# Kernel optimization log

Measured on AMD Instinct MI355X. Metric: run time of the kernel, lower is better.

The kernel has to match this reference:

```python
import jax, jax.numpy as jnp
import numpy as np
from jax import lax

B, S, E, DF, H, L, V, T = 32, 512, 512, 2048, 8, 2, 30000, 12
START, STOP = 10, 11
NEG = -10000.0


def setup_inputs() -> dict:
    key = jax.random.key(0)
    ks = jax.random.split(key, 12)
    g = lambda i, shape, sc=0.02: jax.random.normal(ks[i], shape, jnp.float32) * sc
    trans = jax.random.normal(ks[9], (T, T), jnp.float32)
    trans = trans.at[START, :].set(NEG).at[:, STOP].set(NEG)
    return {
        "sentence": jax.random.randint(ks[0], (B, S), 0, V),
        "seq_len": jax.random.randint(ks[1], (B,), 1, S + 1),
        "tags": jax.random.randint(ks[2], (B, S), 0, 10),
        "emb": g(3, (V, E), 1.0),
        "attn_in_w": g(4, (L, 3 * E, E)), "attn_in_b": jnp.zeros((L, 3 * E)),
        "attn_out_w": g(5, (L, E, E)), "attn_out_b": jnp.zeros((L, E)),
        "ln1_g": jnp.ones((L, E)), "ln1_b": jnp.zeros((L, E)),
        "ln2_g": jnp.ones((L, E)), "ln2_b": jnp.zeros((L, E)),
        "ff1_w": g(6, (L, DF, E)), "ff1_b": jnp.zeros((L, DF)),
        "ff2_w": g(7, (L, E, DF)), "ff2_b": jnp.zeros((L, E)),
        "tag_w": g(8, (T, E)), "tag_b": jnp.zeros((T,)),
        "transitions": trans,
    }


def _ln(x, g, b):
    m = x.mean(-1, keepdims=True)
    v = ((x - m) ** 2).mean(-1, keepdims=True)
    return (x - m) / jnp.sqrt(v + 1e-5) * g + b


def _mha(x, w_in, b_in, w_out, b_out):
    b_, s_, e_ = x.shape
    d = e_ // H
    qkv = x @ w_in.T + b_in
    q, k, v = jnp.split(qkv, 3, axis=-1)
    split = lambda t: t.reshape(b_, s_, H, d).transpose(0, 2, 1, 3)
    q, k, v = split(q), split(k), split(v)
    att = jax.nn.softmax(jnp.einsum('bhqd,bhkd->bhqk', q, k) / np.sqrt(d).astype(np.float32), axis=-1)
    o = jnp.einsum('bhqk,bhkd->bhqd', att, v).transpose(0, 2, 1, 3).reshape(b_, s_, e_)
    return o @ w_out.T + b_out


def _forward_impl(sentence, seq_len, tags, emb, attn_in_w, attn_in_b, attn_out_w,
                  attn_out_b, ln1_g, ln1_b, ln2_g, ln2_b, ff1_w, ff1_b, ff2_w,
                  ff2_b, tag_w, tag_b, transitions):
    # Transformer encoder features (dropout in eval mode -> identity)
    x = emb[sentence]  # (B,S,E)
    for l in range(L):
        x = _ln(x + _mha(x, attn_in_w[l], attn_in_b[l], attn_out_w[l], attn_out_b[l]), ln1_g[l], ln1_b[l])
        h = jax.nn.relu(x @ ff1_w[l].T + ff1_b[l]) @ ff2_w[l].T + ff2_b[l]
        x = _ln(x + h, ln2_g[l], ln2_b[l])
    feats = x @ tag_w.T + tag_b  # (B,S,T)

    # CRF forward algorithm (log-semiring scan, masked by seq_len)
    alpha0 = jnp.full((B, T), NEG, feats.dtype).at[:, START].set(0.0)

    def step(alpha, xs):
        emit_t, t = xs  # emit_t: (B,T)
        new = emit_t + jax.nn.logsumexp(alpha[:, None, :] + transitions[None, :, :], axis=-1)
        return jnp.where((t < seq_len)[:, None], new, alpha), None

    alpha, _ = lax.scan(step, alpha0, (feats.transpose(1, 0, 2), jnp.arange(S)))
    fwd_score = jax.nn.logsumexp(alpha + transitions[STOP][None, :], axis=-1)  # (B,)

    # gold score (vectorized _score_sentence)
    tags_ext = jnp.concatenate([jnp.full((B, 1), START, tags.dtype), tags], axis=1)  # (B,S+1)
    mask = jnp.arange(S)[None, :] < seq_len[:, None]  # (B,S)
    trans_sc = jnp.where(mask, transitions[tags_ext[:, 1:], tags_ext[:, :-1]], 0.0).sum(-1)
    emit_sc = jnp.where(mask, jnp.take_along_axis(feats, tags[:, :, None], axis=2)[..., 0], 0.0).sum(-1)
    last_tag = jnp.take_along_axis(tags_ext, seq_len[:, None], axis=1)[:, 0]
    gold = trans_sc + emit_sc + transitions[STOP, last_tag]

    return jnp.mean(fwd_score - gold)


def reference(sentence, seq_len, tags, emb, attn_in_w, attn_in_b, attn_out_w,
              attn_out_b, ln1_g, ln1_b, ln2_g, ln2_b, ff1_w, ff1_b, ff2_w,
              ff2_b, tag_w, tag_b, transitions):
    return _forward_impl(sentence, seq_len, tags, emb, attn_in_w, attn_in_b,
                         attn_out_w, attn_out_b, ln1_g, ln1_b, ln2_g, ln2_b,
                         ff1_w, ff1_b, ff2_w, ff2_b, tag_w, tag_b, transitions)
```

## Files before the change

kernel.cpp:

```cpp
#include <hip/hip_runtime.h>
#include <hip/hip_bf16.h>

#define BB 32
#define SSZ 512
#define EE 512
#define DFF 2048
#define HH 8
#define LL 2
#define TT 12
#define START_TAG 10
#define STOP_TAG 11
#define CB 8
#define CM (CB * SSZ)
#define NCHUNK (BB / CB)
#define NBH (CB * HH)
#define NBH_ALL (BB * HH)
#define NCHK 8

typedef __hip_bfloat16 bf16;
typedef __attribute__((ext_vector_type(8))) short short8;
typedef __attribute__((ext_vector_type(4))) float f32x4;

__device__ __forceinline__ float b2f(bf16 x) { return __bfloat162float(x); }
__device__ __forceinline__ float ldw(const void* p, size_t i, bool isbf) {
  return isbf ? __bfloat162float(((const bf16*)p)[i]) : ((const float*)p)[i];
}

__device__ __forceinline__ void gl_lds16(const bf16* g, bf16* l) {
  __builtin_amdgcn_global_load_lds(
      (const __attribute__((address_space(1))) void*)g,
      (__attribute__((address_space(3))) void*)l, 16, 0, 0);
}

__device__ __forceinline__ int swz(int row, int col) {
  return row * 128 + (col ^ (((row >> 2) & 7) * 16));
}

__global__ void k_detect(const void* trans, int* dflag) {
  if (threadIdx.x == 0) {
    const unsigned short* u = (const unsigned short*)trans;
    dflag[0] = (u[START_TAG * TT] == 0xC61C && u[START_TAG * TT + 1] == 0xC61C) ? 1 : 0;
  }
}

__global__ void k_cvt(const void* src, bf16* dst, long n, const int* dflag) {
  bool isbf = dflag[0] != 0;
  for (long i = (long)blockIdx.x * 256 + threadIdx.x; i < n; i += (long)gridDim.x * 256)
    dst[i] = __float2bfloat16(ldw(src, i, isbf));
}

__global__ void k_embed(const int* sent, const void* emb, bf16* xb, const int* dflag) {
  bool isbf = dflag[0] != 0;
  int tok = blockIdx.x;
  int v = sent[tok];
  bf16* xo = xb + (size_t)tok * EE;
  for (int i = threadIdx.x; i < EE; i += 256)
    xo[i] = __float2bfloat16(ldw(emb, (size_t)v * EE + i, isbf));
}

__global__ __launch_bounds__(256) void k_mgemm(
    const bf16* __restrict__ A, const bf16* __restrict__ W,
    const void* __restrict__ bias, size_t boff, bf16* __restrict__ Cb,
    bf16* __restrict__ vtout, int M, int N, int K, int relu, const int* dflag) {
  bool isbf = dflag[0] != 0;
  __shared__ __align__(16) bf16 Sh[2 * 128 * 64];
  bf16* As = Sh;
  bf16* Bs = Sh + 128 * 64;
  const int tid = threadIdx.x;
  const int lane = tid & 63;
  const int wave = tid >> 6;
  const int wm = wave >> 1, wn = wave & 1;
  const int m0 = blockIdx.x * 128, n0 = blockIdx.y * 128;
  const int lrow = lane & 15, lk = lane >> 4;
  const int rl = lane >> 3, sl = lane & 7;

  f32x4 acc[4][4];
#pragma unroll
  for (int i = 0; i < 4; ++i)
#pragma unroll
    for (int j = 0; j < 4; ++j) acc[i][j] = (f32x4){0.f, 0.f, 0.f, 0.f};

  for (int kt = 0; kt < K; kt += 64) {
#pragma unroll
    for (int i = 0; i < 4; ++i) {
      int r = wave * 32 + i * 8 + rl;
      int gs = sl ^ (r & 7);
      gl_lds16(A + (size_t)(m0 + r) * K + kt + gs * 8, As + wave * 2048 + i * 512);
      gl_lds16(W + (size_t)(n0 + r) * K + kt + gs * 8, Bs + wave * 2048 + i * 512);
    }
    __syncthreads();
#pragma unroll
    for (int kb = 0; kb < 64; kb += 32) {
      short8 af[4], bfr[4];
#pragma unroll
      for (int mf = 0; mf < 4; ++mf) {
        int r = wm * 64 + mf * 16 + lrow;
        int ps = ((kb >> 3) + lk) ^ (r & 7);
        af[mf] = *(const short8*)&As[r * 64 + ps * 8];
      }
#pragma unroll
      for (int nf = 0; nf < 4; ++nf) {
        int r = wn * 64 + nf * 16 + lrow;
        int ps = ((kb >> 3) + lk) ^ (r & 7);
        bfr[nf] = *(const short8*)&Bs[r * 64 + ps * 8];
      }
#pragma unroll
      for (int mf = 0; mf < 4; ++mf)
#pragma unroll
        for (int nf = 0; nf < 4; ++nf)
          acc[mf][nf] = __builtin_amdgcn_mfma_f32_16x16x32_bf16(
              af[mf], bfr[nf], acc[mf][nf], 0, 0, 0);
    }
    __syncthreads();
  }

  const bool vpath = (vtout != nullptr) && (n0 >= 1024);
  if (!vpath) {
#pragma unroll
    for (int nf = 0; nf < 4; ++nf) {
      int nl = wn * 64 + nf * 16 + lrow;
      float bia = ldw(bias, boff + n0 + nl, isbf);
#pragma unroll
      for (int mf = 0; mf < 4; ++mf) {
#pragma unroll
        for (int r = 0; r < 4; ++r) {
          int ml = wm * 64 + mf * 16 + lk * 4 + r;
          float v = acc[mf][nf][r] + bia;
          if (relu) v = fmaxf(v, 0.f);
          Sh[swz(ml, nl)] = __float2bfloat16(v);
        }
      }
    }
    __syncthreads();
#pragma unroll
    for (int p = 0; p < 8; ++p) {
      int row = p * 16 + (tid >> 4);
      int off = (tid & 15) * 8;
      *(uint4*)(Cb + (size_t)(m0 + row) * N + n0 + off) =
          *(const uint4*)&Sh[swz(row, off)];
    }
  } else {
#pragma unroll
    for (int nf = 0; nf < 4; ++nf) {
      int nl = wn * 64 + nf * 16 + lrow;
      float bia = ldw(bias, boff + n0 + nl, isbf);
#pragma unroll
      for (int mf = 0; mf < 4; ++mf) {
        int mlb = wm * 64 + mf * 16 + lk * 4;
        bf16 t4[4];
#pragma unroll
        for (int r = 0; r < 4; ++r) t4[r] = __float2bfloat16(acc[mf][nf][r] + bia);
        *(uint2*)&Sh[swz(nl, mlb)] = *(const uint2*)t4;
      }
    }
    __syncthreads();
    int h0 = (n0 - 1024) >> 6;
    int blb = (m0 >> 9) * 8;
    int pos0 = m0 & 511;
#pragma unroll
    for (int p = 0; p < 8; ++p) {
      int drow = p * 16 + (tid >> 4);
      int poff = (tid & 15) * 8;
      bf16* dst = vtout + ((size_t)(blb + h0 + (drow >> 6)) * 64 + (drow & 63)) * 512 +
                  pos0 + poff;
      *(uint4*)dst = *(const uint4*)&Sh[swz(drow, poff)];
    }
  }
}

#define LDK 68
#define LDP 72
__global__ __launch_bounds__(256) void k_flash(const bf16* __restrict__ qkv,
                                               const bf16* __restrict__ vt,
                                               bf16* __restrict__ ctx) {
  const int bh = blockIdx.x;
  const int bl = bh >> 3, h = bh & 7;
  const int m0 = blockIdx.y * 128;
  const int tid = threadIdx.x;
  const int lane = tid & 63;
  const int w = tid >> 6;
  const int lrow = lane & 15, lk = lane >> 4;

  __shared__ bf16 Ks[64 * LDK];
  __shared__ bf16 Vs[64 * LDK];
  __shared__ bf16 Ps[4][32 * LDP];

  short8 qf[2][2];
  {
    const bf16* Qb = qkv + (size_t)(bl * SSZ + m0 + w * 32) * 1536 + h * 64;
#pragma unroll
    for (int mf = 0; mf < 2; ++mf)
#pragma unroll
      for (int kb = 0; kb < 2; ++kb)
        qf[mf][kb] = *(const short8*)(Qb + (size_t)(mf * 16 + lrow) * 1536 + kb * 32 + lk * 8);
  }

  f32x4 acc_o[2][4];
  float lsum[2][4];
#pragma unroll
  for (int mf = 0; mf < 2; ++mf) {
#pragma unroll
    for (int nf = 0; nf < 4; ++nf) acc_o[mf][nf] = (f32x4){0.f, 0.f, 0.f, 0.f};
#pragma unroll
    for (int r = 0; r < 4; ++r) lsum[mf][r] = 0.f;
  }

  for (int kt = 0; kt < 8; ++kt) {
#pragma unroll
    for (int i = 0; i < 2; ++i) {
      int cc = tid + i * 256;
      int row = cc >> 3, seg = cc & 7;
      *(uint4*)&Ks[row * LDK + seg * 8] = *(const uint4*)(
          qkv + (size_t)(bl * SSZ + kt * 64 + row) * 1536 + 512 + h * 64 + seg * 8);
      *(uint4*)&Vs[row * LDK + seg * 8] = *(const uint4*)(
          vt + ((size_t)bh * 64 + row) * SSZ + kt * 64 + seg * 8);
    }
    __syncthreads();
    f32x4 s[2][4];
#pragma unroll
    for (int mf = 0; mf < 2; ++mf)
#pragma unroll
      for (int nf = 0; nf < 4; ++nf) s[mf][nf] = (f32x4){0.f, 0.f, 0.f, 0.f};
#pragma unroll
    for (int kb = 0; kb < 2; ++kb) {
      short8 bk[4];
#pragma unroll
      for (int nf = 0; nf < 4; ++nf)
        bk[nf] = *(const short8*)&Ks[(nf * 16 + lrow) * LDK + kb * 32 + lk * 8];
#pragma unroll
      for (int mf = 0; mf < 2; ++mf)
#pragma unroll
        for (int nf = 0; nf < 4; ++nf)
          s[mf][nf] = __builtin_amdgcn_mfma_f32_16x16x32_bf16(qf[mf][kb], bk[nf],
                                                              s[mf][nf], 0, 0, 0);
    }
#pragma unroll
    for (int mf = 0; mf < 2; ++mf)
#pragma unroll
      for (int r = 0; r < 4; ++r) {
        float p0 = __expf(0.125f * s[mf][0][r]);
        float p1 = __expf(0.125f * s[mf][1][r]);
        float p2 = __expf(0.125f * s[mf][2][r]);
        float p3 = __expf(0.125f * s[mf][3][r]);
        s[mf][0][r] = p0; s[mf][1][r] = p1; s[mf][2][r] = p2; s[mf][3][r] = p3;
        lsum[mf][r] += (p0 + p1) + (p2 + p3);
      }
#pragma unroll
    for (int mf = 0; mf < 2; ++mf)
#pragma unroll
      for (int nf = 0; nf < 4; ++nf)
#pragma unroll
        for (int r = 0; r < 4; ++r)
          Ps[w][(mf * 16 + lk * 4 + r) * LDP + nf * 16 + lrow] =
              __float2bfloat16(s[mf][nf][r]);
#pragma unroll
    for (int kb = 0; kb < 2; ++kb) {
      short8 ap[2], bv[4];
#pragma unroll
      for (int mf = 0; mf < 2; ++mf)
        ap[mf] = *(const short8*)&Ps[w][(mf * 16 + lrow) * LDP + kb * 32 + lk * 8];
#pragma unroll
      for (int nf = 0; nf < 4; ++nf)
        bv[nf] = *(const short8*)&Vs[(nf * 16 + lrow) * LDK + kb * 32 + lk * 8];
#pragma unroll
      for (int mf = 0; mf < 2; ++mf)
#pragma unroll
        for (int nf = 0; nf < 4; ++nf)
          acc_o[mf][nf] = __builtin_amdgcn_mfma_f32_16x16x32_bf16(ap[mf], bv[nf],
                                                                  acc_o[mf][nf], 0, 0, 0);
    }
    __syncthreads();
  }
#pragma unroll
  for (int mf = 0; mf < 2; ++mf) {
#pragma unroll
    for (int r = 0; r < 4; ++r) {
      float ls = lsum[mf][r];
      ls += __shfl_xor(ls, 1, 64);
      ls += __shfl_xor(ls, 2, 64);
      ls += __shfl_xor(ls, 4, 64);
      ls += __shfl_xor(ls, 8, 64);
      float inv = 1.f / ls;
      int q = m0 + w * 32 + mf * 16 + lk * 4 + r;
#pragma unroll
      for (int nf = 0; nf < 4; ++nf)
        ctx[((size_t)(bl * SSZ + q)) * EE + h * 64 + nf * 16 + lrow] =
            __float2bfloat16(acc_o[mf][nf][r] * inv);
    }
  }
}

__global__ void k_ln_res(bf16* xb, const bf16* hb, const void* g,
                         const void* be, size_t goff, const int* dflag) {
  bool isbf = dflag[0] != 0;
  int tok = blockIdx.x, tid = threadIdx.x;
  size_t base = (size_t)tok * EE;
  float v0 = b2f(xb[base + tid]) + b2f(hb[base + tid]);
  float v1 = b2f(xb[base + tid + 256]) + b2f(hb[base + tid + 256]);
  float s = v0 + v1, ss = v0 * v0 + v1 * v1;
#pragma unroll
  for (int off = 32; off > 0; off >>= 1) {
    s += __shfl_down(s, off, 64);
    ss += __shfl_down(ss, off, 64);
  }
  __shared__ float ps[4], pss[4];
  __shared__ float mean_s, rstd_s;
  int w = tid >> 6;
  if ((tid & 63) == 0) { ps[w] = s; pss[w] = ss; }
  __syncthreads();
  if (tid == 0) {
    float S_ = ps[0] + ps[1] + ps[2] + ps[3];
    float SS_ = pss[0] + pss[1] + pss[2] + pss[3];
    float mu = S_ / (float)EE;
    float var = SS_ / (float)EE - mu * mu;
    mean_s = mu;
    rstd_s = rsqrtf(var + 1e-5f);
  }
  __syncthreads();
  float mu = mean_s, rs = rstd_s;
  float r0 = (v0 - mu) * rs * ldw(g, goff + tid, isbf) + ldw(be, goff + tid, isbf);
  float r1 = (v1 - mu) * rs * ldw(g, goff + tid + 256, isbf) + ldw(be, goff + tid + 256, isbf);
  xb[base + tid] = __float2bfloat16(r0);
  xb[base + tid + 256] = __float2bfloat16(r1);
}

__global__ void k_feats(const bf16* xb, const bf16* tgw, const void* tgb,
                        float* feats, const int* dflag) {
  bool isbf = dflag[0] != 0;
  int m = blockIdx.x * 4 + (threadIdx.x >> 6);
  int lane = threadIdx.x & 63;
  uint4 raw = *(const uint4*)(xb + (size_t)m * EE + lane * 8);
  const bf16* rb = (const bf16*)&raw;
  float xv[8];
#pragma unroll
  for (int j = 0; j < 8; ++j) xv[j] = b2f(rb[j]);
#pragma unroll
  for (int t = 0; t < TT; ++t) {
    uint4 wraw = *(const uint4*)(tgw + t * EE + lane * 8);
    const bf16* wb = (const bf16*)&wraw;
    float s = 0.f;
#pragma unroll
    for (int j = 0; j < 8; ++j) s += xv[j] * b2f(wb[j]);
#pragma unroll
    for (int off = 32; off > 0; off >>= 1) s += __shfl_down(s, off, 64);
    if (lane == 0) feats[(size_t)m * TT + t] = s + ldw(tgb, t, isbf);
  }
}

__global__ void k_crf1(const float* feats, const int* seq_len, const void* trans_in,
                       float* cmat, const int* dflag) {
  bool isbf = dflag[0] != 0;
  int c = blockIdx.x, b = blockIdx.y;
  int tid = threadIdx.x;
  __shared__ float tr[144];
  __shared__ float abuf[2][144];
  if (tid < 144) tr[tid] = ldw(trans_in, tid, isbf);
  bool act = tid < 144;
  int i = tid / 12, j = tid % 12;
  if (act) abuf[0][tid] = (i == j) ? 0.f : -1e30f;
  __syncthreads();
  float trrow[12];
  if (act) {
#pragma unroll
    for (int k = 0; k < 12; ++k) trrow[k] = tr[i * 12 + k];
  }
  int len = seq_len[b];
  int t0 = c * 64;
  int t1 = min(len, t0 + 64);
  int cur = 0;
  for (int t = t0; t < t1; ++t) {
    float nv = 0.f;
    if (act) {
      float m = -1e30f, v[12];
#pragma unroll
      for (int k = 0; k < 12; ++k) {
        v[k] = trrow[k] + abuf[cur][k * 12 + j];
        m = fmaxf(m, v[k]);
      }
      float s = 0.f;
#pragma unroll
      for (int k = 0; k < 12; ++k) s += __expf(v[k] - m);
      nv = feats[((size_t)b * SSZ + t) * TT + i] + m + __logf(s);
    }
    if (act) abuf[cur ^ 1][tid] = nv;
    __syncthreads();
    cur ^= 1;
  }
  if (act) cmat[((size_t)b * NCHK + c) * 144 + tid] = abuf[cur][tid];
}

__global__ void k_crf2(const float* cmat, const float* feats, const int* tags,
                       const int* seq_len, const void* trans_in, float* bscore,
                       const int* dflag) {
  bool isbf = dflag[0] != 0;
  int b = blockIdx.x;
  int tid = threadIdx.x;
  __shared__ float tr[144];
  __shared__ float tbuf[2][144];
  __shared__ float alpha_sh[12];
  if (tid < 144) tr[tid] = ldw(trans_in, tid, isbf);
  bool act = tid < 144;
  int i = tid / 12, j = tid % 12;
  if (act) tbuf[0][tid] = cmat[((size_t)b * NCHK) * 144 + tid];
  __syncthreads();
  int cur = 0;
  for (int c = 1; c < NCHK; ++c) {
    float nv = 0.f;
    if (act) {
      const float* Cc = cmat + ((size_t)b * NCHK + c) * 144;
      float m = -1e30f, v[12];
#pragma unroll
      for (int k = 0; k < 12; ++k) {
        v[k] = Cc[i * 12 + k] + tbuf[cur][k * 12 + j];
        m = fmaxf(m, v[k]);
      }
      float s = 0.f;
#pragma unroll
      for (int k = 0; k < 12; ++k) s += __expf(v[k] - m);
      nv = m + __logf(s);
    }
    if (act) tbuf[cur ^ 1][tid] = nv;
    __syncthreads();
    cur ^= 1;
  }
  if (tid < 12) {
    float m = -1e30f, v[12];
#pragma unroll
    for (int k = 0; k < 12; ++k) {
      float a0 = (k == START_TAG) ? 0.f : -10000.f;
      v[k] = tbuf[cur][tid * 12 + k] + a0;
      m = fmaxf(m, v[k]);
    }
    float s = 0.f;
#pragma unroll
    for (int k = 0; k < 12; ++k) s += __expf(v[k] - m);
    alpha_sh[tid] = m + __logf(s);
  }
  __syncthreads();
  if (tid < 64) {
    int lane = tid;
    int len = seq_len[b];
    float part = 0.f;
    for (int s = lane; s < len; s += 64) {
      int ct = tags[b * SSZ + s];
      int pv = (s == 0) ? START_TAG : tags[b * SSZ + s - 1];
      part += tr[ct * 12 + pv] + feats[((size_t)b * SSZ + s) * TT + ct];
    }
#pragma unroll
    for (int off = 32; off > 0; off >>= 1) part += __shfl_down(part, off, 64);
    if (lane == 0) {
      float m = -1e30f;
#pragma unroll
      for (int k = 0; k < 12; ++k) m = fmaxf(m, alpha_sh[k] + tr[STOP_TAG * 12 + k]);
      float s = 0.f;
#pragma unroll
      for (int k = 0; k < 12; ++k) s += __expf(alpha_sh[k] + tr[STOP_TAG * 12 + k] - m);
      float fwd = m + __logf(s);
      int last = tags[b * SSZ + len - 1];
      bscore[b] = fwd - (part + tr[STOP_TAG * 12 + last]);
    }
  }
}

__global__ void k_final(const float* bscore, float* out) {
  int tid = threadIdx.x;
  float v = (tid < BB) ? bscore[tid] : 0.f;
#pragma unroll
  for (int off = 32; off > 0; off >>= 1) v += __shfl_down(v, off, 64);
  if (tid == 0) out[0] = v / (float)BB;
}

extern "C" void kernel_launch(void* const* d_in, const int* in_sizes, int n_in,
                              void* d_out, int out_size, void* d_ws, size_t ws_size,
                              hipStream_t stream) {
  const int* sentence = (const int*)d_in[0];
  const int* seq_len = (const int*)d_in[1];
  const int* tags = (const int*)d_in[2];
  const void* emb = d_in[3];
  const void* attn_in_w = d_in[4];
  const void* attn_in_b = d_in[5];
  const void* attn_out_w = d_in[6];
  const void* attn_out_b = d_in[7];
  const void* ln1_g = d_in[8];
  const void* ln1_b = d_in[9];
  const void* ln2_g = d_in[10];
  const void* ln2_b = d_in[11];
  const void* ff1_w = d_in[12];
  const void* ff1_b = d_in[13];
  const void* ff2_w = d_in[14];
  const void* ff2_b = d_in[15];
  const void* tag_w = d_in[16];
  const void* tag_b = d_in[17];
  const void* transitions = d_in[18];

  const int M = BB * SSZ;
  const size_t WEL = (size_t)LL * 3 * EE * EE + (size_t)LL * EE * EE +
                     (size_t)LL * DFF * EE + (size_t)LL * EE * DFF + (size_t)TT * EE;

  size_t o = 0;
  size_t f_feats = o; o += (size_t)M * TT;
  size_t f_bsc = o; o += 64;
  size_t f_cmat = o; o += (size_t)BB * NCHK * 144;
  size_t f_dflag = o; o += 16;
  size_t f_xb = o; o += (size_t)M * EE / 2;
  size_t f_hb = o; o += (size_t)M * EE / 2;
  size_t f_ctxb = o; o += (size_t)M * EE / 2;
  size_t f_act = o; o += (size_t)M * DFF / 2;
  size_t f_vt = o; o += (size_t)NBH_ALL * 64 * SSZ / 2;
  size_t f_w = o; o += (WEL + 1) / 2 + 8;
  size_t need_full = o * 4;
  bool full = ws_size >= need_full;

  float* ws = (float*)d_ws;
  if (full) {
    float* feats = ws + f_feats;
    float* bsc = ws + f_bsc;
    float* cmat = ws + f_cmat;
    int* dflag = (int*)(ws + f_dflag);
    bf16* xb = (bf16*)(ws + f_xb);
    bf16* hb = (bf16*)(ws + f_hb);
    bf16* ctxb = (bf16*)(ws + f_ctxb);
    bf16* act = (bf16*)(ws + f_act);
    bf16* vt = (bf16*)(ws + f_vt);
    bf16* w_aiw = (bf16*)(ws + f_w);
    bf16* w_aow = w_aiw + (size_t)LL * 3 * EE * EE;
    bf16* w_f1 = w_aow + (size_t)LL * EE * EE;
    bf16* w_f2 = w_f1 + (size_t)LL * DFF * EE;
    bf16* w_tg = w_f2 + (size_t)LL * EE * DFF;

    k_detect<<<dim3(1), dim3(64), 0, stream>>>(transitions, dflag);
    k_cvt<<<dim3(1024), dim3(256), 0, stream>>>(attn_in_w, w_aiw, (long)LL * 3 * EE * EE, dflag);
    k_cvt<<<dim3(512), dim3(256), 0, stream>>>(attn_out_w, w_aow, (long)LL * EE * EE, dflag);
    k_cvt<<<dim3(1024), dim3(256), 0, stream>>>(ff1_w, w_f1, (long)LL * DFF * EE, dflag);
    k_cvt<<<dim3(1024), dim3(256), 0, stream>>>(ff2_w, w_f2, (long)LL * EE * DFF, dflag);
    k_cvt<<<dim3(24), dim3(256), 0, stream>>>(tag_w, w_tg, (long)TT * EE, dflag);
    k_embed<<<dim3(M), dim3(256), 0, stream>>>(sentence, emb, xb, dflag);

    for (int l = 0; l < LL; ++l) {
      k_mgemm<<<dim3(M / 128, 12), dim3(256), 0, stream>>>(
          xb, w_aiw + (size_t)l * 3 * EE * EE, attn_in_b, (size_t)l * 3 * EE,
          act, vt, M, 3 * EE, EE, 0, dflag);
      k_flash<<<dim3(NBH_ALL, SSZ / 128), dim3(256), 0, stream>>>(act, vt, ctxb);
      k_mgemm<<<dim3(M / 128, 4), dim3(256), 0, stream>>>(
          ctxb, w_aow + (size_t)l * EE * EE, attn_out_b, (size_t)l * EE,
          hb, (bf16*)nullptr, M, EE, EE, 0, dflag);
      k_ln_res<<<dim3(M), dim3(256), 0, stream>>>(xb, hb, ln1_g, ln1_b,
                                                  (size_t)l * EE, dflag);
      k_mgemm<<<dim3(M / 128, 16), dim3(256), 0, stream>>>(
          xb, w_f1 + (size_t)l * DFF * EE, ff1_b, (size_t)l * DFF,
          act, (bf16*)nullptr, M, DFF, EE, 1, dflag);
      k_mgemm<<<dim3(M / 128, 4), dim3(256), 0, stream>>>(
          act, w_f2 + (size_t)l * EE * DFF, ff2_b, (size_t)l * EE,
          hb, (bf16*)nullptr, M, EE, DFF, 0, dflag);
      k_ln_res<<<dim3(M), dim3(256), 0, stream>>>(xb, hb, ln2_g, ln2_b,
                                                  (size_t)l * EE, dflag);
    }
    k_feats<<<dim3(M / 4), dim3(256), 0, stream>>>(xb, w_tg, tag_b, feats, dflag);
    k_crf1<<<dim3(NCHK, BB), dim3(192), 0, stream>>>(feats, seq_len, transitions, cmat, dflag);
    k_crf2<<<dim3(BB), dim3(192), 0, stream>>>(cmat, feats, tags, seq_len, transitions, bsc, dflag);
    k_final<<<dim3(1), dim3(64), 0, stream>>>(bsc, (float*)d_out);
  } else {
    float* feats = ws;
    float* bsc = feats + (size_t)M * TT;
    float* cmat = bsc + 64;
    int* dflag = (int*)(cmat + (size_t)BB * NCHK * 144 + 16);
    bf16* xb = (bf16*)(dflag + 16);
    bf16* hb = xb + (size_t)M * EE;
    bf16* qkvb = hb + (size_t)CM * EE;
    bf16* ctxb = qkvb + (size_t)CM * 1536;
    bf16* ffh = ctxb + (size_t)CM * EE;
    bf16* vt = ffh + (size_t)CM * DFF;
    bf16* w_aiw = vt + (size_t)NBH * 64 * SSZ;
    bf16* w_aow = w_aiw + (size_t)LL * 3 * EE * EE;
    bf16* w_f1 = w_aow + (size_t)LL * EE * EE;
    bf16* w_f2 = w_f1 + (size_t)LL * DFF * EE;
    bf16* w_tg = w_f2 + (size_t)LL * EE * DFF;

    k_detect<<<dim3(1), dim3(64), 0, stream>>>(transitions, dflag);
    k_cvt<<<dim3(1024), dim3(256), 0, stream>>>(attn_in_w, w_aiw, (long)LL * 3 * EE * EE, dflag);
    k_cvt<<<dim3(512), dim3(256), 0, stream>>>(attn_out_w, w_aow, (long)LL * EE * EE, dflag);
    k_cvt<<<dim3(1024), dim3(256), 0, stream>>>(ff1_w, w_f1, (long)LL * DFF * EE, dflag);
    k_cvt<<<dim3(1024), dim3(256), 0, stream>>>(ff2_w, w_f2, (long)LL * EE * DFF, dflag);
    k_cvt<<<dim3(24), dim3(256), 0, stream>>>(tag_w, w_tg, (long)TT * EE, dflag);
    k_embed<<<dim3(M), dim3(256), 0, stream>>>(sentence, emb, xb, dflag);

    for (int l = 0; l < LL; ++l) {
      for (int c = 0; c < NCHUNK; ++c) {
        bf16* xbc = xb + (size_t)c * CM * EE;
        k_mgemm<<<dim3(CM / 128, 12), dim3(256), 0, stream>>>(
            xbc, w_aiw + (size_t)l * 3 * EE * EE, attn_in_b, (size_t)l * 3 * EE,
            qkvb, vt, CM, 3 * EE, EE, 0, dflag);
        k_flash<<<dim3(NBH, SSZ / 128), dim3(256), 0, stream>>>(qkvb, vt, ctxb);
        k_mgemm<<<dim3(CM / 128, 4), dim3(256), 0, stream>>>(
            ctxb, w_aow + (size_t)l * EE * EE, attn_out_b, (size_t)l * EE,
            hb, (bf16*)nullptr, CM, EE, EE, 0, dflag);
        k_ln_res<<<dim3(CM), dim3(256), 0, stream>>>(xbc, hb, ln1_g, ln1_b,
                                                     (size_t)l * EE, dflag);
        k_mgemm<<<dim3(CM / 128, 16), dim3(256), 0, stream>>>(
            xbc, w_f1 + (size_t)l * DFF * EE, ff1_b, (size_t)l * DFF,
            ffh, (bf16*)nullptr, CM, DFF, EE, 1, dflag);
        k_mgemm<<<dim3(CM / 128, 4), dim3(256), 0, stream>>>(
            ffh, w_f2 + (size_t)l * EE * DFF, ff2_b, (size_t)l * EE,
            hb, (bf16*)nullptr, CM, EE, DFF, 0, dflag);
        k_ln_res<<<dim3(CM), dim3(256), 0, stream>>>(xbc, hb, ln2_g, ln2_b,
                                                     (size_t)l * EE, dflag);
      }
    }
    k_feats<<<dim3(M / 4), dim3(256), 0, stream>>>(xb, w_tg, tag_b, feats, dflag);
    k_crf1<<<dim3(NCHK, BB), dim3(192), 0, stream>>>(feats, seq_len, transitions, cmat, dflag);
    k_crf2<<<dim3(BB), dim3(192), 0, stream>>>(cmat, feats, tags, seq_len, transitions, bsc, dflag);
    k_final<<<dim3(1), dim3(64), 0, stream>>>(bsc, (float*)d_out);
  }
}
```

Before: 711.9 us.

## Replace 128x128 GEMM with double-buffered 256-row tiles and interleaved async loads

```diff
diff --git a/kernel.cpp b/kernel.cpp
--- a/kernel.cpp
+++ b/kernel.cpp
@@ -32,8 +32,20 @@
       (__attribute__((address_space(3))) void*)l, 16, 0, 0);
 }
 
-__device__ __forceinline__ int swz(int row, int col) {
-  return row * 128 + (col ^ (((row >> 2) & 7) * 16));
+__device__ __forceinline__ void stg128(const bf16* __restrict__ G, int ldk,
+                                       int row0, int col0, bf16* lds0,
+                                       int w, int l) {
+#pragma unroll
+  for (int q = 0; q < 2; ++q) {
+    int lr = q * 64 + w * 8 + (l >> 3);
+    int gs = (l & 7) ^ (lr & 7);
+    gl_lds16(G + (size_t)(row0 + lr) * ldk + col0 + gs * 8,
+             lds0 + (q * 64 + w * 8) * 64);
+  }
+}
+
+__device__ __forceinline__ short8 ldfrag(const bf16* T, int row, int gr) {
+  return *(const short8*)&T[row * 64 + ((gr ^ (row & 7)) << 3)];
 }
 
 __global__ void k_detect(const void* trans, int* dflag) {
@@ -58,112 +70,173 @@
     xo[i] = __float2bfloat16(ldw(emb, (size_t)v * EE + i, isbf));
 }
 
-__global__ __launch_bounds__(256) void k_mgemm(
+template <int BN>
+__global__ __launch_bounds__(512, 2) void k_mgemm256(
     const bf16* __restrict__ A, const bf16* __restrict__ W,
     const void* __restrict__ bias, size_t boff, bf16* __restrict__ Cb,
-    bf16* __restrict__ vtout, int M, int N, int K, int relu, const int* dflag) {
-  bool isbf = dflag[0] != 0;
-  __shared__ __align__(16) bf16 Sh[2 * 128 * 64];
-  bf16* As = Sh;
-  bf16* Bs = Sh + 128 * 64;
+    bf16* __restrict__ vtout, int M, int N, int K, int relu,
+    const int* __restrict__ dflag) {
+  constexpr int WN = BN / 64;
+  constexpr int WM = 8 / WN;
+  constexpr int RPW = 256 / WM;
+  constexpr int MFR = RPW / 16;
+  constexpr int QW = MFR / 4;
+  constexpr int BH = BN / 128;
+  constexpr int BUFSZ = 16384 + BN * 64;
+  extern __shared__ __align__(16) bf16 Sh[];
+  const bool isbf = dflag[0] != 0;
   const int tid = threadIdx.x;
-  const int lane = tid & 63;
-  const int wave = tid >> 6;
-  const int wm = wave >> 1, wn = wave & 1;
-  const int m0 = blockIdx.x * 128, n0 = blockIdx.y * 128;
-  const int lrow = lane & 15, lk = lane >> 4;
-  const int rl = lane >> 3, sl = lane & 7;
-
-  f32x4 acc[4][4];
-#pragma unroll
-  for (int i = 0; i < 4; ++i)
+  const int l = tid & 63;
+  const int w = tid >> 6;
+  const int wm = w / WN, wn = w % WN;
+  const int lrow = l & 15, lk = l >> 4;
+  const int m0 = blockIdx.x * 256, n0 = blockIdx.y * BN;
+
+  f32x4 acc[MFR][4];
+#pragma unroll
+  for (int i = 0; i < MFR; ++i)
 #pragma unroll
     for (int j = 0; j < 4; ++j) acc[i][j] = (f32x4){0.f, 0.f, 0.f, 0.f};
 
-  for (int kt = 0; kt < K; kt += 64) {
-#pragma unroll
-    for (int i = 0; i < 4; ++i) {
-      int r = wave * 32 + i * 8 + rl;
-      int gs = sl ^ (r & 7);
-      gl_lds16(A + (size_t)(m0 + r) * K + kt + gs * 8, As + wave * 2048 + i * 512);
-      gl_lds16(W + (size_t)(n0 + r) * K + kt + gs * 8, Bs + wave * 2048 + i * 512);
-    }
-    __syncthreads();
-#pragma unroll
-    for (int kb = 0; kb < 64; kb += 32) {
-      short8 af[4], bfr[4];
-#pragma unroll
-      for (int mf = 0; mf < 4; ++mf) {
-        int r = wm * 64 + mf * 16 + lrow;
-        int ps = ((kb >> 3) + lk) ^ (r & 7);
-        af[mf] = *(const short8*)&As[r * 64 + ps * 8];
+  const int NIT = K >> 7;
+
+#pragma unroll
+  for (int p = 0; p < 2; ++p) {
+    bf16* Ab = Sh + p * BUFSZ;
+    bf16* Bb = Ab + 16384;
+    stg128(A, K, m0, p * 64, Ab, w, l);
+    stg128(A, K, m0 + 128, p * 64, Ab + 8192, w, l);
+#pragma unroll
+    for (int h = 0; h < BH; ++h)
+      stg128(W, K, n0 + h * 128, p * 64, Bb + h * 8192, w, l);
+  }
+  if (BN == 256) asm volatile("s_waitcnt vmcnt(8)" ::: "memory");
+  else asm volatile("s_waitcnt vmcnt(6)" ::: "memory");
+  __builtin_amdgcn_sched_barrier(0);
+  __builtin_amdgcn_s_barrier();
+
+#define LDAQ(q)                                                               \
+  do {                                                                        \
+    _Pragma("unroll") for (int mi = 0; mi < QW; ++mi)                         \
+        _Pragma("unroll") for (int kb = 0; kb < 2; ++kb)                      \
+            aq[q][mi][kb] = ldfrag(                                           \
+                Ab, wm * RPW + ((q)*QW + mi) * 16 + lrow, kb * 4 + lk);       \
+  } while (0)
+
+#define MMQ(q)                                                                \
+  do {                                                                        \
+    __builtin_amdgcn_s_setprio(1);                                            \
+    _Pragma("unroll") for (int mi = 0; mi < QW; ++mi)                         \
+        _Pragma("unroll") for (int kb = 0; kb < 2; ++kb)                      \
+            _Pragma("unroll") for (int nf = 0; nf < 4; ++nf)                  \
+                acc[(q)*QW + mi][nf] =                                        \
+                    __builtin_amdgcn_mfma_f32_16x16x32_bf16(                  \
+                        aq[q][mi][kb], bfr[kb][nf], acc[(q)*QW + mi][nf],     \
+                        0, 0, 0);                                             \
+    __builtin_amdgcn_s_setprio(0);                                            \
+  } while (0)
+
+#pragma unroll 1
+  for (int i = 0; i < NIT; ++i) {
+    const bool more = (i + 1 < NIT);
+#pragma unroll
+    for (int hh = 0; hh < 2; ++hh) {
+      bf16* Ab = Sh + hh * BUFSZ;
+      bf16* Bb = Ab + 16384;
+      const int kc2 = (2 * i + 2 + hh) << 6;
+      short8 bfr[2][4];
+      short8 aq[4][QW][2];
+#pragma unroll
+      for (int kb = 0; kb < 2; ++kb)
+#pragma unroll
+        for (int nf = 0; nf < 4; ++nf)
+          bfr[kb][nf] = ldfrag(Bb, wn * 64 + nf * 16 + lrow, kb * 4 + lk);
+      LDAQ(0);
+      MMQ(0);
+      __builtin_amdgcn_s_barrier();
+      LDAQ(1);
+      LDAQ(2);
+      MMQ(1);
+      __builtin_amdgcn_s_barrier();
+      LDAQ(3);
+      if (more) {
+#pragma unroll
+        for (int h = 0; h < BH; ++h)
+          stg128(W, K, n0 + h * 128, kc2, Bb + h * 8192, w, l);
       }
-#pragma unroll
-      for (int nf = 0; nf < 4; ++nf) {
-        int r = wn * 64 + nf * 16 + lrow;
-        int ps = ((kb >> 3) + lk) ^ (r & 7);
-        bfr[nf] = *(const short8*)&Bs[r * 64 + ps * 8];
+      MMQ(2);
+      asm volatile("s_waitcnt lgkmcnt(0)" ::: "memory");
+      __builtin_amdgcn_sched_barrier(0);
+      __builtin_amdgcn_s_barrier();
+      if (more) {
+        stg128(A, K, m0, kc2, Ab, w, l);
+        stg128(A, K, m0 + 128, kc2, Ab + 8192, w, l);
       }
-#pragma unroll
-      for (int mf = 0; mf < 4; ++mf)
-#pragma unroll
-        for (int nf = 0; nf < 4; ++nf)
-          acc[mf][nf] = __builtin_amdgcn_mfma_f32_16x16x32_bf16(
-              af[mf], bfr[nf], acc[mf][nf], 0, 0, 0);
-    }
-    __syncthreads();
-  }
-
-  const bool vpath = (vtout != nullptr) && (n0 >= 1024);
+      MMQ(3);
+      if (more) {
+        if (BN == 256) asm volatile("s_waitcnt vmcnt(8)" ::: "memory");
+        else asm volatile("s_waitcnt vmcnt(6)" ::: "memory");
+      } else {
+        asm volatile("s_waitcnt vmcnt(0)" ::: "memory");
+      }
+      __builtin_amdgcn_sched_barrier(0);
+      __builtin_amdgcn_s_barrier();
+    }
+  }
+#undef LDAQ
+#undef MMQ
+
+  const bool vpath = (BN == 256) && (vtout != nullptr) && (n0 >= 1024);
   if (!vpath) {
 #pragma unroll
     for (int nf = 0; nf < 4; ++nf) {
-      int nl = wn * 64 + nf * 16 + lrow;
-      float bia = ldw(bias, boff + n0 + nl, isbf);
-#pragma unroll
-      for (int mf = 0; mf < 4; ++mf) {
+      const int c = wn * 64 + nf * 16 + lrow;
+      const float bia = ldw(bias, boff + n0 + c, isbf);
+#pragma unroll
+      for (int mf = 0; mf < MFR; ++mf)
 #pragma unroll
         for (int r = 0; r < 4; ++r) {
-          int ml = wm * 64 + mf * 16 + lk * 4 + r;
+          const int row = wm * RPW + mf * 16 + lk * 4 + r;
           float v = acc[mf][nf][r] + bia;
           if (relu) v = fmaxf(v, 0.f);
-          Sh[swz(ml, nl)] = __float2bfloat16(v);
+          Sh[row * BN + (c ^ (((row >> 2) & 7) << 4))] = __float2bfloat16(v);
         }
-      }
     }
     __syncthreads();
-#pragma unroll
-    for (int p = 0; p < 8; ++p) {
-      int row = p * 16 + (tid >> 4);
-      int off = (tid & 15) * 8;
-      *(uint4*)(Cb + (size_t)(m0 + row) * N + n0 + off) =
-          *(const uint4*)&Sh[swz(row, off)];
+    constexpr int GPR = BN / 8;
+    constexpr int RPP = 512 / GPR;
+#pragma unroll
+    for (int p = 0; p < 256 / RPP; ++p) {
+      const int row = p * RPP + tid / GPR;
+      const int g = tid % GPR;
+      *(uint4*)(Cb + (size_t)(m0 + row) * N + n0 + g * 8) =
+          *(const uint4*)&Sh[row * BN + ((g * 8) ^ (((row >> 2) & 7) << 4))];
     }
   } else {
+    const int pos0 = m0 & 511;
+    const int blb = (m0 >> 9) * 8;
 #pragma unroll
     for (int nf = 0; nf < 4; ++nf) {
-      int nl = wn * 64 + nf * 16 + lrow;
-      float bia = ldw(bias, boff + n0 + nl, isbf);
-#pragma unroll
-      for (int mf = 0; mf < 4; ++mf) {
-        int mlb = wm * 64 + mf * 16 + lk * 4;
-        bf16 t4[4];
-#pragma unroll
-        for (int r = 0; r < 4; ++r) t4[r] = __float2bfloat16(acc[mf][nf][r] + bia);
-        *(uint2*)&Sh[swz(nl, mlb)] = *(const uint2*)t4;
-      }
+      const int c = wn * 64 + nf * 16 + lrow;
+      const float bia = ldw(bias, boff + n0 + c, isbf);
+#pragma unroll
+      for (int mf = 0; mf < MFR; ++mf)
+#pragma unroll
+        for (int r = 0; r < 4; ++r) {
+          const int row = wm * RPW + mf * 16 + lk * 4 + r;
+          Sh[c * 256 + (row ^ (((c >> 2) & 7) << 4))] =
+              __float2bfloat16(acc[mf][nf][r] + bia);
+        }
     }
     __syncthreads();
-    int h0 = (n0 - 1024) >> 6;
-    int blb = (m0 >> 9) * 8;
-    int pos0 = m0 & 511;
-#pragma unroll
-    for (int p = 0; p < 8; ++p) {
-      int drow = p * 16 + (tid >> 4);
-      int poff = (tid & 15) * 8;
-      bf16* dst = vtout + ((size_t)(blb + h0 + (drow >> 6)) * 64 + (drow & 63)) * 512 +
-                  pos0 + poff;
-      *(uint4*)dst = *(const uint4*)&Sh[swz(drow, poff)];
+#pragma unroll
+    for (int p = 0; p < 16; ++p) {
+      const int cc = p * 16 + (tid >> 5);
+      const int g = tid & 31;
+      const int vc = n0 - 1024 + cc;
+      *(uint4*)(vtout + ((size_t)(blb + (vc >> 6)) * 64 + (vc & 63)) * 512 +
+                pos0 + g * 8) =
+          *(const uint4*)&Sh[cc * 256 + ((g * 8) ^ (((cc >> 2) & 7) << 4))];
     }
   }
 }
@@ -493,6 +566,15 @@
   const void* tag_b = d_in[17];
   const void* transitions = d_in[18];
 
+  static int attr_done = 0;
+  if (!attr_done) {
+    (void)hipFuncSetAttribute((const void*)&k_mgemm256<256>,
+                              hipFuncAttributeMaxDynamicSharedMemorySize, 131072);
+    (void)hipFuncSetAttribute((const void*)&k_mgemm256<128>,
+                              hipFuncAttributeMaxDynamicSharedMemorySize, 131072);
+    attr_done = 1;
+  }
+
   const int M = BB * SSZ;
   const size_t WEL = (size_t)LL * 3 * EE * EE + (size_t)LL * EE * EE +
                      (size_t)LL * DFF * EE + (size_t)LL * EE * DFF + (size_t)TT * EE;
@@ -537,19 +619,19 @@
     k_embed<<<dim3(M), dim3(256), 0, stream>>>(sentence, emb, xb, dflag);
 
     for (int l = 0; l < LL; ++l) {
-      k_mgemm<<<dim3(M / 128, 12), dim3(256), 0, stream>>>(
+      k_mgemm256<256><<<dim3(M / 256, 6), dim3(512), 131072, stream>>>(
           xb, w_aiw + (size_t)l * 3 * EE * EE, attn_in_b, (size_t)l * 3 * EE,
           act, vt, M, 3 * EE, EE, 0, dflag);
       k_flash<<<dim3(NBH_ALL, SSZ / 128), dim3(256), 0, stream>>>(act, vt, ctxb);
-      k_mgemm<<<dim3(M / 128, 4), dim3(256), 0, stream>>>(
+      k_mgemm256<128><<<dim3(M / 256, EE / 128), dim3(512), 98304, stream>>>(
           ctxb, w_aow + (size_t)l * EE * EE, attn_out_b, (size_t)l * EE,
           hb, (bf16*)nullptr, M, EE, EE, 0, dflag);
       k_ln_res<<<dim3(M), dim3(256), 0, stream>>>(xb, hb, ln1_g, ln1_b,
                                                   (size_t)l * EE, dflag);
-      k_mgemm<<<dim3(M / 128, 16), dim3(256), 0, stream>>>(
+      k_mgemm256<256><<<dim3(M / 256, DFF / 256), dim3(512), 131072, stream>>>(
           xb, w_f1 + (size_t)l * DFF * EE, ff1_b, (size_t)l * DFF,
           act, (bf16*)nullptr, M, DFF, EE, 1, dflag);
-      k_mgemm<<<dim3(M / 128, 4), dim3(256), 0, stream>>>(
+      k_mgemm256<128><<<dim3(M / 256, EE / 128), dim3(512), 98304, stream>>>(
           act, w_f2 + (size_t)l * EE * DFF, ff2_b, (size_t)l * EE,
           hb, (bf16*)nullptr, M, EE, DFF, 0, dflag);
       k_ln_res<<<dim3(M), dim3(256), 0, stream>>>(xb, hb, ln2_g, ln2_b,
@@ -587,19 +669,19 @@
     for (int l = 0; l < LL; ++l) {
       for (int c = 0; c < NCHUNK; ++c) {
         bf16* xbc = xb + (size_t)c * CM * EE;
-        k_mgemm<<<dim3(CM / 128, 12), dim3(256), 0, stream>>>(
+        k_mgemm256<256><<<dim3(CM / 256, 6), dim3(512), 131072, stream>>>(
             xbc, w_aiw + (size_t)l * 3 * EE * EE, attn_in_b, (size_t)l * 3 * EE,
             qkvb, vt, CM, 3 * EE, EE, 0, dflag);
         k_flash<<<dim3(NBH, SSZ / 128), dim3(256), 0, stream>>>(qkvb, vt, ctxb);
-        k_mgemm<<<dim3(CM / 128, 4), dim3(256), 0, stream>>>(
+        k_mgemm256<128><<<dim3(CM / 256, EE / 128), dim3(512), 98304, stream>>>(
             ctxb, w_aow + (size_t)l * EE * EE, attn_out_b, (size_t)l * EE,
             hb, (bf16*)nullptr, CM, EE, EE, 0, dflag);
         k_ln_res<<<dim3(CM), dim3(256), 0, stream>>>(xbc, hb, ln1_g, ln1_b,
                                                      (size_t)l * EE, dflag);
-        k_mgemm<<<dim3(CM / 128, 16), dim3(256), 0, stream>>>(
+        k_mgemm256<256><<<dim3(CM / 256, DFF / 256), dim3(512), 131072, stream>>>(
             xbc, w_f1 + (size_t)l * DFF * EE, ff1_b, (size_t)l * DFF,
             ffh, (bf16*)nullptr, CM, DFF, EE, 1, dflag);
-        k_mgemm<<<dim3(CM / 128, 4), dim3(256), 0, stream>>>(
+        k_mgemm256<128><<<dim3(CM / 256, EE / 128), dim3(512), 98304, stream>>>(
             ffh, w_f2 + (size_t)l * EE * DFF, ff2_b, (size_t)l * EE,
             hb, (bf16*)nullptr, CM, EE, DFF, 0, dflag);
         k_ln_res<<<dim3(CM), dim3(256), 0, stream>>>(xbc, hb, ln2_g, ln2_b,
```

Result: faster. 696.9 us (-2.1%).
